# Performance work log

Measured on AMD Instinct MI355X. Metric: run time of the kernel, lower is better.

The kernel has to match this reference:

```python
import jax, jax.numpy as jnp
import numpy as np

B, D0, D1, D2 = 512, 4096, 4096, 4096
W_SCALE = 0.01  # small init so sigmoids stay in a useful range


def setup_inputs() -> dict:
    key = jax.random.key(0)
    k0, k1, k2, k3, k4 = jax.random.split(key, 5)
    return {
        "data": jax.random.uniform(k0, (B, D0), dtype=jnp.float32),
        "W1": jax.random.normal(k1, (D0, D1), dtype=jnp.float32) * W_SCALE,
        "W2": jax.random.normal(k2, (D1, D2), dtype=jnp.float32) * W_SCALE,
        "b1": jax.random.normal(k3, (D1,), dtype=jnp.float32),
        "b2": jax.random.normal(k4, (D2,), dtype=jnp.float32),
        "iterations": 10,
    }


def reference(data, W1, W2, b1, b2, iterations):
    """Mean-field conditional sample of a 3-layer DBM (visible clamped to data).

    Faithful to conditional_sample_general_meanfield with mean_cond (sigmoid
    of bias + interaction), sample_state[0]=False, invtemperature=1.0.
    Schedule per iteration: odd layers (j=1) then even layers (j=2).
    """
    beta = jnp.float32(1.0)
    nb = data.shape[0]
    # initial states: layer mean activations broadcast over the batch
    s1 = jnp.broadcast_to(jax.nn.sigmoid(b1), (nb, b1.shape[0]))
    s2 = jnp.broadcast_to(jax.nn.sigmoid(b2), (nb, b2.shape[0]))

    def gibbs_step(carry, _):
        s1, s2 = carry
        # j=1: interaction from below (gradOutput: data @ W1) and above (gradInput: s2 @ W2^T)
        s1 = jax.nn.sigmoid(b1 + beta * (data @ W1 + s2 @ W2.T))
        # j=2: interaction from below (gradOutput: s1 @ W2); j=0 clamped
        s2 = jax.nn.sigmoid(b2 + beta * (s1 @ W2))
        return (s1, s2), None

    (s1, s2), _ = jax.lax.scan(gibbs_step, (s1, s2), None, length=iterations)
    # original returns [state0, state1, state2]; state0 == data (clamped)
    return jnp.stack([s1, s2])  # [2, B, D]
```

## Files before the change

### kernel.cpp

```cpp
#include <hip/hip_runtime.h>


typedef __bf16 bf16_t;
typedef __attribute__((ext_vector_type(8))) __bf16 bf16x8;
typedef __attribute__((ext_vector_type(4))) __bf16 bf16x4;
typedef __attribute__((ext_vector_type(4))) float f32x4;
typedef __attribute__((ext_vector_type(2))) _Float16 half2v;
typedef __attribute__((ext_vector_type(8))) _Float16 f16x8;

typedef const __attribute__((address_space(1))) void* gptr_t;
typedef __attribute__((address_space(3))) void* lptr_t;

constexpr int M = 512, N = 4096, K = 4096;
constexpr int BM = 256, BN = 256, BK = 64;
constexpr int SPLIT = 8;
constexpr int KSLICE = K / SPLIT;
constexpr int KTILES = KSLICE / BK;
constexpr int NTILES = (M / BM) * (N / BN);
constexpr int TILE_H2 = BM * BN / 2;
constexpr int PLANE = 256 * 32;


__global__ __launch_bounds__(256) void prep_w(const float* __restrict__ in,
                                              bf16_t* __restrict__ outT,
                                              bf16_t* __restrict__ outC) {
  __shared__ float t[64][65];
  const int tid = threadIdx.x;
  const int x0 = blockIdx.x * 64, y0 = blockIdx.y * 64;
  const int row = tid >> 4;
  const int xs  = tid & 15;
#pragma unroll
  for (int i = 0; i < 4; ++i) {
    const int r = row + 16 * i;
    float4 v = *(const float4*)(in + (size_t)(y0 + r) * 4096 + x0 + xs * 4);
    t[xs * 4 + 0][r] = v.x;
    t[xs * 4 + 1][r] = v.y;
    t[xs * 4 + 2][r] = v.z;
    t[xs * 4 + 3][r] = v.w;
  }
  __syncthreads();
#pragma unroll
  for (int j = 0; j < 2; ++j) {
    const int idx = tid + 256 * j;
    const int xr = idx >> 3, sg = idx & 7;
    bf16x8 v;
#pragma unroll
    for (int e = 0; e < 8; ++e) v[e] = (bf16_t)t[xr][sg * 8 + e];
    *(bf16x8*)(outT + (size_t)(x0 + xr) * 4096 + y0 + sg * 8) = v;
  }
  if (outC) {
#pragma unroll
    for (int j = 0; j < 2; ++j) {
      const int idx = tid + 256 * j;
      const int yr = idx >> 3, sg = idx & 7;
      bf16x8 v;
#pragma unroll
      for (int e = 0; e < 8; ++e) v[e] = (bf16_t)t[sg * 8 + e][yr];
      *(bf16x8*)(outC + (size_t)(y0 + yr) * 4096 + x0 + sg * 8) = v;
    }
  }
}

__global__ __launch_bounds__(256) void cvt_bf16(const float* __restrict__ in,
                                                bf16_t* __restrict__ out) {
  const size_t i8 = ((size_t)blockIdx.x * 256 + threadIdx.x) * 8;
  float4 a = *(const float4*)(in + i8);
  float4 b = *(const float4*)(in + i8 + 4);
  bf16x8 o;
  o[0] = (bf16_t)a.x; o[1] = (bf16_t)a.y; o[2] = (bf16_t)a.z; o[3] = (bf16_t)a.w;
  o[4] = (bf16_t)b.x; o[5] = (bf16_t)b.y; o[6] = (bf16_t)b.z; o[7] = (bf16_t)b.w;
  *(bf16x8*)(out + i8) = o;
}

__global__ __launch_bounds__(256) void init_s2(const float* __restrict__ b2,
                                               bf16_t* __restrict__ s2, int total) {
  int i = blockIdx.x * 256 + threadIdx.x;
  if (i < total) {
    float x = b2[i & (N - 1)];
    s2[i] = (bf16_t)(1.0f / (1.0f + __expf(-x)));
  }
}

__global__ __launch_bounds__(512, 2) void gemm_bt(
    const bf16_t* __restrict__ A,
    const bf16_t* __restrict__ BT,
    _Float16* __restrict__ slabs) {
  __shared__ __align__(16) bf16_t lds[8 * PLANE];

  const int gid = blockIdx.x;
  const int z = gid & 7;
  const int rem = gid >> 3;
  const int tx = rem & 15;
  const int ty = rem >> 4;
  const int tile = ty * 16 + tx;

  const int tid = threadIdx.x;
  const int wid = tid >> 6;
  const int l   = tid & 63;
  const int r   = l & 15;
  const int q   = l >> 4;
  const int wm  = wid & 1;
  const int wn  = wid >> 1;

  const bf16_t* Ab = A + (size_t)(ty * BM) * K + (size_t)z * KSLICE;
  const bf16_t* Bb = BT + (size_t)(tx * BN) * K + (size_t)z * KSLICE;

  const int srow = l >> 2;
  const int scol = ((l & 3) ^ ((l >> 3) & 3)) * 8;

  const int pq = (q ^ ((r >> 1) & 3)) * 8;

  auto plane = [&](int b, int mat, int kk) -> bf16_t* {
    return lds + ((size_t)((b * 2 + mat) * 2 + kk)) * PLANE;
  };

  auto stage = [&](int tt, int kk) {
    const int b = tt & 1;
    const size_t kof = (size_t)tt * BK + kk * 32;
#pragma unroll
    for (int i = 0; i < 2; ++i) {
      const int ch = wid * 2 + i;
      const int row = ch * 16 + srow;
      __builtin_amdgcn_global_load_lds(
          (gptr_t)(Ab + (size_t)row * K + kof + scol),
          (lptr_t)(plane(b, 0, kk) + ch * 512), 16, 0, 0);
    }
#pragma unroll
    for (int i = 0; i < 2; ++i) {
      const int ch = wid * 2 + i;
      const int row = ch * 16 + srow;
      __builtin_amdgcn_global_load_lds(
          (gptr_t)(Bb + (size_t)row * K + kof + scol),
          (lptr_t)(plane(b, 1, kk) + ch * 512), 16, 0, 0);
    }
  };

  f32x4 acc[8][4];
  const f32x4 zero = {0.0f, 0.0f, 0.0f, 0.0f};
#pragma unroll
  for (int i = 0; i < 8; ++i)
#pragma unroll
    for (int j = 0; j < 4; ++j) acc[i][j] = zero;

#define MMA_CLUSTER(AF, MB)                                                  \
  __builtin_amdgcn_s_setprio(1);                                             \
  _Pragma("unroll") for (int mt = 0; mt < 4; ++mt)                           \
      _Pragma("unroll") for (int nt = 0; nt < 4; ++nt)                       \
          acc[(MB) + mt][nt] = __builtin_amdgcn_mfma_f32_16x16x32_bf16(      \
              AF[mt], bfr[nt], acc[(MB) + mt][nt], 0, 0, 0);                 \
  __builtin_amdgcn_s_setprio(0);

  stage(0, 0);
  stage(0, 1);
  asm volatile("s_waitcnt vmcnt(4)" ::: "memory");
  __builtin_amdgcn_s_barrier();
  __builtin_amdgcn_sched_barrier(0);

  for (int t = 0; t < KTILES; ++t) {
    const int b = t & 1;
    const bf16_t* pA0 = plane(b, 0, 0);
    const bf16_t* pA1 = plane(b, 0, 1);
    const bf16_t* pB0 = plane(b, 1, 0);
    const bf16_t* pB1 = plane(b, 1, 1);
    const int arow0 = (wm * 128 + r) * 32 + pq;
    const int brow  = (wn * 64 + r) * 32 + pq;

    {
      bf16x8 bfr[4], af0[4], af1[4];
#pragma unroll
      for (int nt = 0; nt < 4; ++nt)
        bfr[nt] = *(const bf16x8*)(pB0 + brow + nt * (16 * 32));
#pragma unroll
      for (int mt = 0; mt < 4; ++mt)
        af0[mt] = *(const bf16x8*)(pA0 + arow0 + mt * (16 * 32));
      if (t + 1 < KTILES) stage(t + 1, 0);
      MMA_CLUSTER(af0, 0)
#pragma unroll
      for (int mt = 0; mt < 4; ++mt)
        af1[mt] = *(const bf16x8*)(pA0 + arow0 + (64 * 32) + mt * (16 * 32));
      MMA_CLUSTER(af1, 4)
    }
    if (t + 1 < KTILES)
      asm volatile("s_waitcnt vmcnt(4)" ::: "memory");
    else
      asm volatile("s_waitcnt vmcnt(0)" ::: "memory");
    __builtin_amdgcn_s_barrier();
    __builtin_amdgcn_sched_barrier(0);

    {
      bf16x8 bfr[4], af0[4], af1[4];
#pragma unroll
      for (int nt = 0; nt < 4; ++nt)
        bfr[nt] = *(const bf16x8*)(pB1 + brow + nt * (16 * 32));
#pragma unroll
      for (int mt = 0; mt < 4; ++mt)
        af0[mt] = *(const bf16x8*)(pA1 + arow0 + mt * (16 * 32));
      if (t + 1 < KTILES) stage(t + 1, 1);
      MMA_CLUSTER(af0, 0)
#pragma unroll
      for (int mt = 0; mt < 4; ++mt)
        af1[mt] = *(const bf16x8*)(pA1 + arow0 + (64 * 32) + mt * (16 * 32));
      MMA_CLUSTER(af1, 4)
    }
    if (t + 1 < KTILES) {
      asm volatile("s_waitcnt vmcnt(4)" ::: "memory");
      __builtin_amdgcn_s_barrier();
      __builtin_amdgcn_sched_barrier(0);
    }
  }
#undef MMA_CLUSTER

  half2v* P2 = (half2v*)slabs + ((size_t)z * NTILES + tile) * TILE_H2;
#pragma unroll
  for (int mt = 0; mt < 8; ++mt)
#pragma unroll
    for (int nt = 0; nt < 4; ++nt)
#pragma unroll
      for (int i2 = 0; i2 < 2; ++i2) {
        half2v h;
        h[0] = (_Float16)acc[mt][nt][2 * i2];
        h[1] = (_Float16)acc[mt][nt][2 * i2 + 1];
        __builtin_nontemporal_store(
            h, P2 + (size_t)((((wid * 8 + mt) * 4 + nt) * 2 + i2) * 64 + l));
      }
}

template <int MODE>
__global__ __launch_bounds__(256) void epi(const _Float16* __restrict__ slabs,
                                           const float* __restrict__ bias,
                                           const bf16_t* __restrict__ C0b,
                                           bf16_t* __restrict__ outb,
                                           float* __restrict__ outf) {
  const int g = blockIdx.x * 256 + threadIdx.x;
  const int tile = g >> 13;
  const int gi = g & 8191;
  const int slot = gi >> 4;
  const int l4 = (gi & 15) * 4;

  float s0[4] = {0.f, 0.f, 0.f, 0.f};
  float s1[4] = {0.f, 0.f, 0.f, 0.f};
  const size_t ubase = (size_t)tile * TILE_H2 + slot * 64 + l4;
#pragma unroll
  for (int zz = 0; zz < SPLIT; ++zz) {
    f16x8 v = *(const f16x8*)((const half2v*)slabs +
                              (size_t)zz * NTILES * TILE_H2 + ubase);
#pragma unroll
    for (int j = 0; j < 4; ++j) {
      s0[j] += (float)v[2 * j];
      s1[j] += (float)v[2 * j + 1];
    }
  }

  const int i2 = slot & 1, nt = (slot >> 1) & 3, mt = (slot >> 3) & 7,
            wid = slot >> 6;
  const int wm = wid & 1, wn = wid >> 1;
  const int q = (gi & 15) >> 2, rb = (gi & 3) * 4;
  const int ty = tile >> 4, tx = tile & 15;
  const int row = ty * 256 + wm * 128 + mt * 16 + q * 4 + 2 * i2;
  const int col = tx * 256 + wn * 64 + nt * 16 + rb;
  const size_t i0 = (size_t)row * N + col;
  const size_t i1 = i0 + N;

  if (MODE == 0) {
    bf16x4 o0, o1;
#pragma unroll
    for (int j = 0; j < 4; ++j) { o0[j] = (bf16_t)s0[j]; o1[j] = (bf16_t)s1[j]; }
    *(bf16x4*)(outb + i0) = o0;
    *(bf16x4*)(outb + i1) = o1;
    return;
  }
  const float4 bv = *(const float4*)(bias + col);
  s0[0] += bv.x; s0[1] += bv.y; s0[2] += bv.z; s0[3] += bv.w;
  s1[0] += bv.x; s1[1] += bv.y; s1[2] += bv.z; s1[3] += bv.w;
  if (MODE == 1) {
    bf16x4 c0 = *(const bf16x4*)(C0b + i0);
    bf16x4 c1 = *(const bf16x4*)(C0b + i1);
#pragma unroll
    for (int j = 0; j < 4; ++j) { s0[j] += (float)c0[j]; s1[j] += (float)c1[j]; }
  }
  float v0[4], v1[4];
  bf16x4 o0, o1;
#pragma unroll
  for (int j = 0; j < 4; ++j) {
    v0[j] = 1.0f / (1.0f + __expf(-s0[j]));
    v1[j] = 1.0f / (1.0f + __expf(-s1[j]));
    o0[j] = (bf16_t)v0[j];
    o1[j] = (bf16_t)v1[j];
  }
  *(bf16x4*)(outb + i0) = o0;
  *(bf16x4*)(outb + i1) = o1;
  if (outf) {
    float4 f0 = {v0[0], v0[1], v0[2], v0[3]};
    float4 f1 = {v1[0], v1[1], v1[2], v1[3]};
    *(float4*)(outf + i0) = f0;
    *(float4*)(outf + i1) = f1;
  }
}


extern "C" void kernel_launch(void* const* d_in, const int* in_sizes, int n_in,
                              void* d_out, int out_size, void* d_ws, size_t ws_size,
                              hipStream_t stream) {
  const float* data = (const float*)d_in[0];
  const float* W1   = (const float*)d_in[1];
  const float* W2   = (const float*)d_in[2];
  const float* b1   = (const float*)d_in[3];
  const float* b2   = (const float*)d_in[4];

  char* p = (char*)d_ws;
  bf16_t* W1T = (bf16_t*)p; p += (size_t)K * N * 2;
  bf16_t* W2b = (bf16_t*)p; p += (size_t)K * N * 2;
  bf16_t* W2T = (bf16_t*)p; p += (size_t)K * N * 2;
  bf16_t* C0b = (bf16_t*)p; p += (size_t)M * N * 2;
  bf16_t* s1b = (bf16_t*)p; p += (size_t)M * N * 2;
  bf16_t* s2b = (bf16_t*)p; p += (size_t)M * N * 2;
  bf16_t* dat = (bf16_t*)p; p += (size_t)M * K * 2;

  _Float16* slabC = (_Float16*)W2T;
  _Float16* slab  = (_Float16*)W1T;

  float* out_s1 = (float*)d_out;
  float* out_s2 = out_s1 + (size_t)M * N;

  cvt_bf16<<<(M * K) / 2048, 256, 0, stream>>>(data, dat);
  prep_w<<<dim3(64, 64), 256, 0, stream>>>(W1, W1T, (bf16_t*)nullptr);

  const int gblocks = NTILES * SPLIT;
  const int epiblocks = (M * N / 8) / 256;

  gemm_bt<<<gblocks, 512, 0, stream>>>(dat, W1T, slabC);
  epi<0><<<epiblocks, 256, 0, stream>>>(slabC, nullptr, nullptr, C0b, nullptr);

  prep_w<<<dim3(64, 64), 256, 0, stream>>>(W2, W2T, W2b);
  init_s2<<<(M * N) / 256, 256, 0, stream>>>(b2, s2b, M * N);

  for (int it = 0; it < 10; ++it) {
    const bool last = (it == 9);
    gemm_bt<<<gblocks, 512, 0, stream>>>(s2b, W2b, slab);
    epi<1><<<epiblocks, 256, 0, stream>>>(slab, b1, C0b, s1b,
                                          last ? out_s1 : (float*)nullptr);
    gemm_bt<<<gblocks, 512, 0, stream>>>(s1b, W2T, slab);
    epi<2><<<epiblocks, 256, 0, stream>>>(slab, b2, nullptr, s2b,
                                          last ? out_s2 : (float*)nullptr);
  }
}
```

Before: 768.1 us.

## Fuse split-K reduction and sigmoid epilogue into GEMM via last-block atomic counter

```diff
diff --git a/kernel.cpp b/kernel.cpp
--- a/kernel.cpp
+++ b/kernel.cpp
@@ -7,6 +7,7 @@
 typedef __attribute__((ext_vector_type(4))) float f32x4;
 typedef __attribute__((ext_vector_type(2))) _Float16 half2v;
 typedef __attribute__((ext_vector_type(8))) _Float16 f16x8;
+typedef __attribute__((ext_vector_type(4))) int int4v;
 
 typedef const __attribute__((address_space(1))) void* gptr_t;
 typedef __attribute__((address_space(3))) void* lptr_t;
@@ -62,7 +63,9 @@
 }
 
 __global__ __launch_bounds__(256) void cvt_bf16(const float* __restrict__ in,
-                                                bf16_t* __restrict__ out) {
+                                                bf16_t* __restrict__ out,
+                                                unsigned* __restrict__ cnt) {
+  if (blockIdx.x == 0 && threadIdx.x < NTILES) cnt[threadIdx.x] = 0u;
   const size_t i8 = ((size_t)blockIdx.x * 256 + threadIdx.x) * 8;
   float4 a = *(const float4*)(in + i8);
   float4 b = *(const float4*)(in + i8 + 4);
@@ -81,11 +84,18 @@
   }
 }
 
-__global__ __launch_bounds__(512, 2) void gemm_bt(
+template <int MODE>
+__global__ __launch_bounds__(512, 2) void gemm_fused(
     const bf16_t* __restrict__ A,
     const bf16_t* __restrict__ BT,
-    _Float16* __restrict__ slabs) {
+    _Float16* __restrict__ slabs,
+    unsigned* __restrict__ cnt,
+    const float* __restrict__ bias,
+    const bf16_t* __restrict__ C0b,
+    bf16_t* __restrict__ outb,
+    float* __restrict__ outf) {
   __shared__ __align__(16) bf16_t lds[8 * PLANE];
+  __shared__ int isLast;
 
   const int gid = blockIdx.x;
   const int z = gid & 7;
@@ -220,80 +230,121 @@
         half2v h;
         h[0] = (_Float16)acc[mt][nt][2 * i2];
         h[1] = (_Float16)acc[mt][nt][2 * i2 + 1];
-        __builtin_nontemporal_store(
-            h, P2 + (size_t)((((wid * 8 + mt) * 4 + nt) * 2 + i2) * 64 + l));
-      }
-}
-
-template <int MODE>
-__global__ __launch_bounds__(256) void epi(const _Float16* __restrict__ slabs,
-                                           const float* __restrict__ bias,
-                                           const bf16_t* __restrict__ C0b,
-                                           bf16_t* __restrict__ outb,
-                                           float* __restrict__ outf) {
-  const int g = blockIdx.x * 256 + threadIdx.x;
-  const int tile = g >> 13;
-  const int gi = g & 8191;
-  const int slot = gi >> 4;
-  const int l4 = (gi & 15) * 4;
-
-  float s0[4] = {0.f, 0.f, 0.f, 0.f};
-  float s1[4] = {0.f, 0.f, 0.f, 0.f};
-  const size_t ubase = (size_t)tile * TILE_H2 + slot * 64 + l4;
-#pragma unroll
-  for (int zz = 0; zz < SPLIT; ++zz) {
-    f16x8 v = *(const f16x8*)((const half2v*)slabs +
-                              (size_t)zz * NTILES * TILE_H2 + ubase);
-#pragma unroll
-    for (int j = 0; j < 4; ++j) {
-      s0[j] += (float)v[2 * j];
-      s1[j] += (float)v[2 * j + 1];
-    }
-  }
-
-  const int i2 = slot & 1, nt = (slot >> 1) & 3, mt = (slot >> 3) & 7,
-            wid = slot >> 6;
-  const int wm = wid & 1, wn = wid >> 1;
-  const int q = (gi & 15) >> 2, rb = (gi & 3) * 4;
-  const int ty = tile >> 4, tx = tile & 15;
-  const int row = ty * 256 + wm * 128 + mt * 16 + q * 4 + 2 * i2;
-  const int col = tx * 256 + wn * 64 + nt * 16 + rb;
-  const size_t i0 = (size_t)row * N + col;
-  const size_t i1 = i0 + N;
-
-  if (MODE == 0) {
-    bf16x4 o0, o1;
-#pragma unroll
-    for (int j = 0; j < 4; ++j) { o0[j] = (bf16_t)s0[j]; o1[j] = (bf16_t)s1[j]; }
-    *(bf16x4*)(outb + i0) = o0;
-    *(bf16x4*)(outb + i1) = o1;
-    return;
-  }
-  const float4 bv = *(const float4*)(bias + col);
-  s0[0] += bv.x; s0[1] += bv.y; s0[2] += bv.z; s0[3] += bv.w;
-  s1[0] += bv.x; s1[1] += bv.y; s1[2] += bv.z; s1[3] += bv.w;
-  if (MODE == 1) {
-    bf16x4 c0 = *(const bf16x4*)(C0b + i0);
-    bf16x4 c1 = *(const bf16x4*)(C0b + i1);
-#pragma unroll
-    for (int j = 0; j < 4; ++j) { s0[j] += (float)c0[j]; s1[j] += (float)c1[j]; }
-  }
-  float v0[4], v1[4];
-  bf16x4 o0, o1;
-#pragma unroll
-  for (int j = 0; j < 4; ++j) {
-    v0[j] = 1.0f / (1.0f + __expf(-s0[j]));
-    v1[j] = 1.0f / (1.0f + __expf(-s1[j]));
-    o0[j] = (bf16_t)v0[j];
-    o1[j] = (bf16_t)v1[j];
-  }
-  *(bf16x4*)(outb + i0) = o0;
-  *(bf16x4*)(outb + i1) = o1;
-  if (outf) {
-    float4 f0 = {v0[0], v0[1], v0[2], v0[3]};
-    float4 f1 = {v1[0], v1[1], v1[2], v1[3]};
-    *(float4*)(outf + i0) = f0;
-    *(float4*)(outf + i1) = f1;
+        half2v* ad = P2 + (size_t)((((wid * 8 + mt) * 4 + nt) * 2 + i2) * 64 + l);
+        asm volatile("global_store_dword %0, %1, off sc1"
+                     :: "v"(ad), "v"(__builtin_bit_cast(int, h)) : "memory");
+      }
+
+  asm volatile("s_waitcnt vmcnt(0)" ::: "memory");
+  __syncthreads();
+  if (tid == 0) {
+    unsigned old = __hip_atomic_fetch_add(cnt + tile, 1u, __ATOMIC_RELAXED,
+                                          __HIP_MEMORY_SCOPE_AGENT);
+    int last = (old == SPLIT - 1);
+    if (last)
+      __hip_atomic_store(cnt + tile, 0u, __ATOMIC_RELAXED,
+                         __HIP_MEMORY_SCOPE_AGENT);
+    isLast = last;
+  }
+  __syncthreads();
+  if (!isLast) return;
+
+  int4v buf[2][8];
+#pragma unroll
+  for (int gg = 0; gg < 16; ++gg) {
+    const int pb = gg & 1;
+    if (gg == 0) {
+      const int gi = tid;
+      const size_t base = (size_t)tile * TILE_H2 + (size_t)(gi >> 4) * 64 +
+                          (gi & 15) * 4;
+#pragma unroll
+      for (int zz = 0; zz < 8; ++zz) {
+        const half2v* ad =
+            (const half2v*)slabs + (size_t)zz * (NTILES * TILE_H2) + base;
+        asm volatile("global_load_dwordx4 %0, %1, off sc1"
+                     : "=v"(buf[0][zz]) : "v"(ad) : "memory");
+      }
+    }
+    if (gg + 1 < 16) {
+      const int gi = (gg + 1) * 512 + tid;
+      const size_t base = (size_t)tile * TILE_H2 + (size_t)(gi >> 4) * 64 +
+                          (gi & 15) * 4;
+#pragma unroll
+      for (int zz = 0; zz < 8; ++zz) {
+        const half2v* ad =
+            (const half2v*)slabs + (size_t)zz * (NTILES * TILE_H2) + base;
+        asm volatile("global_load_dwordx4 %0, %1, off sc1"
+                     : "=v"(buf[pb ^ 1][zz]) : "v"(ad) : "memory");
+      }
+      asm volatile("s_waitcnt vmcnt(8)" ::: "memory");
+    } else {
+      asm volatile("s_waitcnt vmcnt(0)" ::: "memory");
+    }
+    __builtin_amdgcn_sched_barrier(0);
+
+    float a0[4] = {0.f, 0.f, 0.f, 0.f};
+    float a1[4] = {0.f, 0.f, 0.f, 0.f};
+#pragma unroll
+    for (int zz = 0; zz < 8; ++zz) {
+      f16x8 v = __builtin_bit_cast(f16x8, buf[pb][zz]);
+#pragma unroll
+      for (int j = 0; j < 4; ++j) {
+        a0[j] += (float)v[2 * j];
+        a1[j] += (float)v[2 * j + 1];
+      }
+    }
+
+    const int gi = gg * 512 + tid;
+    const int slot = gi >> 4;
+    const int i2 = slot & 1, ntd = (slot >> 1) & 3, mtd = (slot >> 3) & 7,
+              wd = slot >> 6;
+    const int wmm = wd & 1, wnn = wd >> 1;
+    const int qd = (gi & 15) >> 2, rb = (gi & 3) * 4;
+    const int row = ty * 256 + wmm * 128 + mtd * 16 + qd * 4 + 2 * i2;
+    const int col = tx * 256 + wnn * 64 + ntd * 16 + rb;
+    const size_t i0 = (size_t)row * N + col;
+    const size_t i1 = i0 + N;
+
+    if (MODE == 0) {
+      bf16x4 o0, o1;
+#pragma unroll
+      for (int j = 0; j < 4; ++j) {
+        o0[j] = (bf16_t)a0[j];
+        o1[j] = (bf16_t)a1[j];
+      }
+      *(bf16x4*)(outb + i0) = o0;
+      *(bf16x4*)(outb + i1) = o1;
+    } else {
+      const float4 bv = *(const float4*)(bias + col);
+      a0[0] += bv.x; a0[1] += bv.y; a0[2] += bv.z; a0[3] += bv.w;
+      a1[0] += bv.x; a1[1] += bv.y; a1[2] += bv.z; a1[3] += bv.w;
+      if (MODE == 1) {
+        bf16x4 c0 = *(const bf16x4*)(C0b + i0);
+        bf16x4 c1 = *(const bf16x4*)(C0b + i1);
+#pragma unroll
+        for (int j = 0; j < 4; ++j) {
+          a0[j] += (float)c0[j];
+          a1[j] += (float)c1[j];
+        }
+      }
+      float v0[4], v1[4];
+      bf16x4 o0, o1;
+#pragma unroll
+      for (int j = 0; j < 4; ++j) {
+        v0[j] = 1.0f / (1.0f + __expf(-a0[j]));
+        v1[j] = 1.0f / (1.0f + __expf(-a1[j]));
+        o0[j] = (bf16_t)v0[j];
+        o1[j] = (bf16_t)v1[j];
+      }
+      *(bf16x4*)(outb + i0) = o0;
+      *(bf16x4*)(outb + i1) = o1;
+      if (outf) {
+        float4 f0 = {v0[0], v0[1], v0[2], v0[3]};
+        float4 f1 = {v1[0], v1[1], v1[2], v1[3]};
+        *(float4*)(outf + i0) = f0;
+        *(float4*)(outf + i1) = f1;
+      }
+    }
   }
 }
 
@@ -315,6 +366,7 @@
   bf16_t* s1b = (bf16_t*)p; p += (size_t)M * N * 2;
   bf16_t* s2b = (bf16_t*)p; p += (size_t)M * N * 2;
   bf16_t* dat = (bf16_t*)p; p += (size_t)M * K * 2;
+  unsigned* cnt = (unsigned*)p; p += 128;
 
   _Float16* slabC = (_Float16*)W2T;
   _Float16* slab  = (_Float16*)W1T;
@@ -322,25 +374,22 @@
   float* out_s1 = (float*)d_out;
   float* out_s2 = out_s1 + (size_t)M * N;
 
-  cvt_bf16<<<(M * K) / 2048, 256, 0, stream>>>(data, dat);
+  cvt_bf16<<<(M * K) / 2048, 256, 0, stream>>>(data, dat, cnt);
   prep_w<<<dim3(64, 64), 256, 0, stream>>>(W1, W1T, (bf16_t*)nullptr);
 
   const int gblocks = NTILES * SPLIT;
-  const int epiblocks = (M * N / 8) / 256;
-
-  gemm_bt<<<gblocks, 512, 0, stream>>>(dat, W1T, slabC);
-  epi<0><<<epiblocks, 256, 0, stream>>>(slabC, nullptr, nullptr, C0b, nullptr);
+
+  gemm_fused<0><<<gblocks, 512, 0, stream>>>(dat, W1T, slabC, cnt, nullptr,
+                                             nullptr, C0b, nullptr);
 
   prep_w<<<dim3(64, 64), 256, 0, stream>>>(W2, W2T, W2b);
   init_s2<<<(M * N) / 256, 256, 0, stream>>>(b2, s2b, M * N);
 
   for (int it = 0; it < 10; ++it) {
     const bool last = (it == 9);
-    gemm_bt<<<gblocks, 512, 0, stream>>>(s2b, W2b, slab);
-    epi<1><<<epiblocks, 256, 0, stream>>>(slab, b1, C0b, s1b,
-                                          last ? out_s1 : (float*)nullptr);
-    gemm_bt<<<gblocks, 512, 0, stream>>>(s1b, W2T, slab);
-    epi<2><<<epiblocks, 256, 0, stream>>>(slab, b2, nullptr, s2b,
-                                          last ? out_s2 : (float*)nullptr);
-  }
-}
+    gemm_fused<1><<<gblocks, 512, 0, stream>>>(
+        s2b, W2b, slab, cnt, b1, C0b, s1b, last ? out_s1 : (float*)nullptr);
+    gemm_fused<2><<<gblocks, 512, 0, stream>>>(
+        s1b, W2T, slab, cnt, b2, nullptr, s2b, last ? out_s2 : (float*)nullptr);
+  }
+}
```

Result: slower. 1.202 ms (+56.4%).
